# Performance work log

Measured on AMD Instinct MI355X. Metric: run time of the kernel, lower is better.

## Reference

```python
import jax, jax.numpy as jnp
import numpy as np

N = 50000      # nodes
E = 800000     # edges
H = 64         # hid_dim (== in_dim)
T = 4          # number of S2V message-passing steps


def setup_inputs() -> dict:
    key = jax.random.key(0)
    ks = jax.random.split(key, 12)
    mu = jax.random.normal(ks[0], (N, H), dtype=jnp.float32)
    x = jax.random.uniform(ks[1], (N, 1), dtype=jnp.float32)
    edge_index = jax.random.randint(ks[2], (2, E), 0, N, dtype=jnp.int64)
    edge_w = jax.random.uniform(ks[3], (E, 1), dtype=jnp.float32)
    s = 0.05  # small init scale to keep activations bounded across T relu layers
    W1 = jax.random.normal(ks[4], (T, H, 1), dtype=jnp.float32) * s   # lin1 per layer, torch [out,in]
    W2 = jax.random.normal(ks[5], (T, H, H), dtype=jnp.float32) * s   # lin2 per layer
    W3 = jax.random.normal(ks[6], (T, H, H), dtype=jnp.float32) * s   # lin3 per layer
    W4 = jax.random.normal(ks[7], (T, H, 1), dtype=jnp.float32) * s   # lin4 per layer
    W5 = jax.random.normal(ks[8], (1, 2 * H), dtype=jnp.float32) * s  # lin5
    W7 = jax.random.normal(ks[9], (H, H), dtype=jnp.float32) * s      # lin7
    return {"mu": mu, "x": x, "edge_index": edge_index, "edge_w": edge_w,
            "W1": W1, "W2": W2, "W3": W3, "W4": W4, "W5": W5, "W7": W7}


def _s2v_step(mu, x, idx, edge_w, w1, w2, w3, w4):
    # Faithful to source: gather AND scatter both use edge_index[1].
    x_emb = x @ w1.T                                            # [N,H]
    mu_j = mu[idx]                                              # [E,H] gather
    mu_aggr = jax.ops.segment_sum(mu_j, idx, num_segments=N)    # [N,H] scatter_add
    mu_aggr = mu_aggr @ w2.T
    ew = jax.nn.relu(edge_w @ w4.T)                             # [E,H]
    ew_aggr = jax.ops.segment_sum(ew, idx, num_segments=N)      # [N,H]
    ew_aggr = ew_aggr @ w3.T
    return jax.nn.relu(x_emb + mu_aggr + ew_aggr)


def reference(mu, x, edge_index, edge_w, W1, W2, W3, W4, W5, W7):
    idx = edge_index[1]
    for t in range(T):
        mu = _s2v_step(mu, x, idx, edge_w, W1[t], W2[t], W3[t], W4[t])
    nodes_vec = mu @ W7.T                                       # [N,H]
    graph_pool = jnp.broadcast_to(jnp.sum(mu, axis=0, keepdims=True), (N, H))
    cat = jnp.concatenate([graph_pool, nodes_vec], axis=1)      # [N,2H]
    return (jax.nn.relu(cat) @ W5.T).squeeze(-1)                # [N]
```

## Files before the change

kernel.cpp:

```cpp
#include <hip/hip_runtime.h>

#define H 64
#define NPB 64
#define KS 104
typedef short bf16x8 __attribute__((ext_vector_type(8)));
typedef float f32x4 __attribute__((ext_vector_type(4)));

static __device__ __forceinline__ unsigned short f2bf(float f) {
    union { float f; unsigned u; } v; v.f = f;
    unsigned r = v.u + 0x7fffu + ((v.u >> 16) & 1u);
    return (unsigned short)(r >> 16);
}
static __device__ __forceinline__ float bf2f(unsigned short b) {
    union { unsigned u; float f; } v; v.u = ((unsigned)b) << 16;
    return v.f;
}
static __device__ __forceinline__ void split8(const float* ff, bf16x8& hi, bf16x8& lo) {
#pragma unroll
    for (int j = 0; j < 8; ++j) {
        unsigned short h = f2bf(ff[j]);
        hi[j] = (short)h;
        lo[j] = (short)f2bf(ff[j] - bf2f(h));
    }
}


__global__ __launch_bounds__(256)
void edge_prep_kernel(const int* __restrict__ ei, const float* __restrict__ ew,
                      const float* __restrict__ W1, const float* __restrict__ W2,
                      const float* __restrict__ W3, const float* __restrict__ W4,
                      const float* __restrict__ W7, float* __restrict__ dSf,
                      bf16x8* __restrict__ Bp, bf16x8* __restrict__ W7p, int E) {
    __shared__ float v3s[256];
    const int t = threadIdx.x;
    const int bid = blockIdx.x;

    if (bid == 0) {
        {
            int tl = t >> 6, h2 = t & 63;
            const float* __restrict__ w3r = W3 + (tl * H + h2) * H;
            const float* __restrict__ w4r = W4 + tl * H;
            float a0 = 0, a1 = 0, a2 = 0, a3 = 0;
#pragma unroll
            for (int k = 0; k < H; k += 4) {
                a0 += fmaxf(w4r[k + 0], 0.f) * w3r[k + 0];
                a1 += fmaxf(w4r[k + 1], 0.f) * w3r[k + 1];
                a2 += fmaxf(w4r[k + 2], 0.f) * w3r[k + 2];
                a3 += fmaxf(w4r[k + 3], 0.f) * w3r[k + 3];
            }
            v3s[t] = (a0 + a1) + (a2 + a3);
        }
        __syncthreads();
        const int w = t >> 6, lane = t & 63, c = lane & 15, q = lane >> 4;
        const int hh = 16 * w + c;
        for (int tl = 0; tl < 4; ++tl) {
            const int b3 = (tl * 4 + w) * 3;
            bf16x8 hi, lo;
#pragma unroll
            for (int s = 0; s < 2; ++s) {
                const float* __restrict__ wp = W2 + (tl * H + hh) * H + s * 32 + q * 8;
                float4 f0 = *(const float4*)(wp);
                float4 f1 = *(const float4*)(wp + 4);
                float ff[8] = {f0.x, f0.y, f0.z, f0.w, f1.x, f1.y, f1.z, f1.w};
                split8(ff, hi, lo);
                Bp[(b3 + s) * 128 + lane] = hi;
                Bp[(b3 + s) * 128 + 64 + lane] = lo;
            }
            float ff[8] = {0, 0, 0, 0, 0, 0, 0, 0};
            if (q == 0) { ff[0] = W1[tl * H + hh]; ff[1] = v3s[tl * H + hh]; }
            split8(ff, hi, lo);
            Bp[(b3 + 2) * 128 + lane] = hi;
            Bp[(b3 + 2) * 128 + 64 + lane] = lo;
        }
#pragma unroll
        for (int s = 0; s < 2; ++s) {
            const float* __restrict__ wp = W7 + hh * H + s * 32 + q * 8;
            float4 f0 = *(const float4*)(wp);
            float4 f1 = *(const float4*)(wp + 4);
            float ff[8] = {f0.x, f0.y, f0.z, f0.w, f1.x, f1.y, f1.z, f1.w};
            bf16x8 hi, lo;
            split8(ff, hi, lo);
            W7p[(w * 2 + s) * 128 + lane] = hi;
            W7p[(w * 2 + s) * 128 + 64 + lane] = lo;
        }
        return;
    }

    int probe = ei[2 * (t & 63) + 1];
    bool is64 = (__ballot(probe != 0) == 0ULL);
    const int base_e = 8 * ((bid - 1) * 256 + t);
#pragma unroll
    for (int g = 0; g < 2; ++g) {
        int e0 = base_e + 4 * g;
        if (e0 + 3 < E) {
            float4 wv = *(const float4*)(ew + e0);
            int i0, i1, i2, i3;
            if (is64) {
                int4 a = *(const int4*)(ei + 2 * (E + e0));
                int4 b = *(const int4*)(ei + 2 * (E + e0) + 4);
                i0 = a.x; i1 = a.z; i2 = b.x; i3 = b.z;
            } else {
                int4 a = *(const int4*)(ei + E + e0);
                i0 = a.x; i1 = a.y; i2 = a.z; i3 = a.w;
            }
            unsafeAtomicAdd(&dSf[i0], 4096.0f + wv.x);
            unsafeAtomicAdd(&dSf[i1], 4096.0f + wv.y);
            unsafeAtomicAdd(&dSf[i2], 4096.0f + wv.z);
            unsafeAtomicAdd(&dSf[i3], 4096.0f + wv.w);
        } else {
            for (int j = 0; j < 4 && e0 + j < E; ++j) {
                int e = e0 + j;
                int idx = is64 ? ei[2 * (E + e)] : ei[E + e];
                unsafeAtomicAdd(&dSf[idx], 4096.0f + ew[e]);
            }
        }
    }
}

__global__ __launch_bounds__(256, 4)
void node_kernel(const float* __restrict__ mu, const float* __restrict__ x,
                 const float* __restrict__ W5, const bf16x8* __restrict__ Bp,
                 const bf16x8* __restrict__ W7p, const float* __restrict__ dSf,
                 float* __restrict__ gp, float* __restrict__ out, int N) {
    __shared__ unsigned short Ab[2][NPB * KS];
    __shared__ float degs[NPB];
    __shared__ float red[4 * NPB];

    const int t = threadIdx.x;
    const int lane = t & 63;
    const int w = __builtin_amdgcn_readfirstlane(t >> 6);
    const int c = lane & 15;
    const int q = lane >> 4;
    const int hh = 16 * w + c;
    const int base = blockIdx.x * NPB;

    if (t < 128) {
        int buf = t >> 6, row = t & 63;
        unsigned* p = (unsigned*)&Ab[buf][row * KS];
#pragma unroll
        for (int d = 33; d < 52; ++d) p[d] = 0u;
    }
    if (t < 64) {
        int node = base + t;
        float dg = 0.f, sv = 0.f, xv = 0.f;
        if (node < N) {
            float T = dSf[node];
            float k = floorf(T * (1.0f / 4096.0f));
            dg = k;
            sv = T - 4096.0f * k;
            xv = x[node];
        }
        degs[t] = dg;
        unsigned short xb = f2bf(xv), sb = f2bf(sv);
        Ab[0][t * KS + 64] = xb; Ab[0][t * KS + 65] = sb;
        Ab[1][t * KS + 64] = xb; Ab[1][t * KS + 65] = sb;
    }
    __syncthreads();

    {
        const float* __restrict__ mublk = mu + (size_t)base * H;
        const int maxf = (N - base) * H;
#pragma unroll
        for (int cc = 0; cc < 4; ++cc) {
            int f = (t + 256 * cc) * 4;
            float4 v = make_float4(0.f, 0.f, 0.f, 0.f);
            if (f < maxf) v = *(const float4*)(mublk + f);
            int m = f >> 6, k = f & 63;
            float dg = degs[m];
            ushort4 b;
            b.x = f2bf(v.x * dg); b.y = f2bf(v.y * dg);
            b.z = f2bf(v.z * dg); b.w = f2bf(v.w * dg);
            *(ushort4*)(&Ab[0][m * KS + k]) = b;
        }
    }
    __syncthreads();

    unsigned short* Acur = &Ab[0][0];
    unsigned short* Anxt = &Ab[1][0];

    for (int tl = 0; tl < 4; ++tl) {
        const int b3 = (tl * 4 + w) * 3;
        bf16x8 bh0 = Bp[(b3 + 0) * 128 + lane], bl0 = Bp[(b3 + 0) * 128 + 64 + lane];
        bf16x8 bh1 = Bp[(b3 + 1) * 128 + lane], bl1 = Bp[(b3 + 1) * 128 + 64 + lane];
        bf16x8 bh2 = Bp[(b3 + 2) * 128 + lane], bl2 = Bp[(b3 + 2) * 128 + 64 + lane];

        f32x4 acc[4];
#pragma unroll
        for (int mt = 0; mt < 4; ++mt)
#pragma unroll
            for (int r = 0; r < 4; ++r) acc[mt][r] = 0.f;

#pragma unroll
        for (int mt = 0; mt < 4; ++mt) {
            const unsigned short* ar = Acur + (mt * 16 + c) * KS;
            bf16x8 a0 = *(const bf16x8*)(ar + q * 8);
            bf16x8 a1 = *(const bf16x8*)(ar + 32 + q * 8);
            bf16x8 a2 = *(const bf16x8*)(ar + 64 + q * 8);
            acc[mt] = __builtin_amdgcn_mfma_f32_16x16x32_bf16(a0, bh0, acc[mt], 0, 0, 0);
            acc[mt] = __builtin_amdgcn_mfma_f32_16x16x32_bf16(a0, bl0, acc[mt], 0, 0, 0);
            acc[mt] = __builtin_amdgcn_mfma_f32_16x16x32_bf16(a1, bh1, acc[mt], 0, 0, 0);
            acc[mt] = __builtin_amdgcn_mfma_f32_16x16x32_bf16(a1, bl1, acc[mt], 0, 0, 0);
            acc[mt] = __builtin_amdgcn_mfma_f32_16x16x32_bf16(a2, bh2, acc[mt], 0, 0, 0);
            acc[mt] = __builtin_amdgcn_mfma_f32_16x16x32_bf16(a2, bl2, acc[mt], 0, 0, 0);
        }

        const bool scale = (tl < 3);
#pragma unroll
        for (int mt = 0; mt < 4; ++mt) {
#pragma unroll
            for (int r = 0; r < 4; ++r) {
                int m = mt * 16 + q * 4 + r;
                float v = fmaxf(acc[mt][r], 0.f);
                if (scale) v *= degs[m];
                Anxt[m * KS + hh] = f2bf(v);
            }
        }
        __syncthreads();
        unsigned short* tmp = Acur; Acur = Anxt; Anxt = tmp;
    }

    {
        bf16x8 bh0 = W7p[(w * 2 + 0) * 128 + lane], bl0 = W7p[(w * 2 + 0) * 128 + 64 + lane];
        bf16x8 bh1 = W7p[(w * 2 + 1) * 128 + lane], bl1 = W7p[(w * 2 + 1) * 128 + 64 + lane];
        f32x4 acc[4];
#pragma unroll
        for (int mt = 0; mt < 4; ++mt)
#pragma unroll
            for (int r = 0; r < 4; ++r) acc[mt][r] = 0.f;
#pragma unroll
        for (int mt = 0; mt < 4; ++mt) {
            const unsigned short* ar = Acur + (mt * 16 + c) * KS;
            bf16x8 a0 = *(const bf16x8*)(ar + q * 8);
            bf16x8 a1 = *(const bf16x8*)(ar + 32 + q * 8);
            acc[mt] = __builtin_amdgcn_mfma_f32_16x16x32_bf16(a0, bh0, acc[mt], 0, 0, 0);
            acc[mt] = __builtin_amdgcn_mfma_f32_16x16x32_bf16(a0, bl0, acc[mt], 0, 0, 0);
            acc[mt] = __builtin_amdgcn_mfma_f32_16x16x32_bf16(a1, bh1, acc[mt], 0, 0, 0);
            acc[mt] = __builtin_amdgcn_mfma_f32_16x16x32_bf16(a1, bl1, acc[mt], 0, 0, 0);
        }
        float w5v = W5[H + hh];
#pragma unroll
        for (int mt = 0; mt < 4; ++mt) {
#pragma unroll
            for (int r = 0; r < 4; ++r) {
                float v = fmaxf(acc[mt][r], 0.f) * w5v;
                v += __shfl_xor(v, 1);
                v += __shfl_xor(v, 2);
                v += __shfl_xor(v, 4);
                v += __shfl_xor(v, 8);
                if (c == 0) red[w * 64 + mt * 16 + q * 4 + r] = v;
            }
        }
    }
    __syncthreads();
    if (t < 64) {
        float pn = red[t] + red[64 + t] + red[128 + t] + red[192 + t];
        if (base + t < N) out[base + t] = pn;
    }
    __syncthreads();

    {
        int h2 = t & 63, mq = t >> 6;
        float s = 0.f;
#pragma unroll
        for (int i = 0; i < 16; ++i) s += bf2f(Acur[(mq * 16 + i) * KS + h2]);
        red[t] = s;
    }
    __syncthreads();
    if (t < 64) {
        float g = red[t] + red[64 + t] + red[128 + t] + red[192 + t];
        unsafeAtomicAdd(&gp[t], g);
    }
}

__global__ __launch_bounds__(256)
void finalize_kernel(const float* __restrict__ gp, const float* __restrict__ W5,
                     float* __restrict__ out, int N) {
    int lane = threadIdx.x & 63;
    float v = fmaxf(gp[lane], 0.f) * W5[lane];
    v += __shfl_xor(v, 1);
    v += __shfl_xor(v, 2);
    v += __shfl_xor(v, 4);
    v += __shfl_xor(v, 8);
    v += __shfl_xor(v, 16);
    v += __shfl_xor(v, 32);
    int n = blockIdx.x * blockDim.x + threadIdx.x;
    if (n < N) out[n] += v;
}

extern "C" void kernel_launch(void* const* d_in, const int* in_sizes, int n_in,
                              void* d_out, int out_size, void* d_ws, size_t ws_size,
                              hipStream_t stream) {
    const float* mu = (const float*)d_in[0];
    const float* x  = (const float*)d_in[1];
    const int*   ei = (const int*)d_in[2];
    const float* ew = (const float*)d_in[3];
    const float* W1 = (const float*)d_in[4];
    const float* W2 = (const float*)d_in[5];
    const float* W3 = (const float*)d_in[6];
    const float* W4 = (const float*)d_in[7];
    const float* W5 = (const float*)d_in[8];
    const float* W7 = (const float*)d_in[9];
    float* out = (float*)d_out;

    const int N = in_sizes[1];
    const int E = in_sizes[3];

    char* ws = (char*)d_ws;
    float*  dSf = (float*)ws;
    float*  gp  = (float*)(ws + (size_t)N * 4);
    bf16x8* Bp  = (bf16x8*)(ws + (size_t)N * 4 + 256);
    bf16x8* W7p = (bf16x8*)(ws + (size_t)N * 4 + 256 + 196608);

    hipMemsetAsync(ws, 0, (size_t)N * 4 + 256, stream);

    int nb_e = 1 + (E + 8 * 256 - 1) / (8 * 256);
    edge_prep_kernel<<<nb_e, 256, 0, stream>>>(ei, ew, W1, W2, W3, W4, W7,
                                               dSf, Bp, W7p, E);
    node_kernel<<<(N + NPB - 1) / NPB, 256, 0, stream>>>(mu, x, W5, Bp, W7p,
                                                         dSf, gp, out, N);
    finalize_kernel<<<(N + 255) / 256, 256, 0, stream>>>(gp, W5, out, N);
}
```

Baseline: 154.5 us.

## Keep node activations in registers with transposed MFMA, drop shared-memory staging

The node kernel now computes the transposed product (weights times activations), so each wave keeps its own 16 nodes' activations in MFMA B-operand registers across all four layers. Activations are re-laid out between layers with lane shuffles instead of being written to LDS and reloaded behind a block barrier. The x*W1 and edge-weight terms are applied as scalar FMAs in the epilogue rather than as a third K-slice of the MFMA, which removes two MFMAs per tile. This cuts LDS traffic, block barriers and the LDS footprint, at the cost of more shuffles, more registers, and repeated small global loads of W1/v3 per layer.

```diff
diff --git a/kernel.cpp b/kernel.cpp
--- a/kernel.cpp
+++ b/kernel.cpp
@@ -2,7 +2,6 @@
 
 #define H 64
 #define NPB 64
-#define KS 104
 typedef short bf16x8 __attribute__((ext_vector_type(8)));
 typedef float f32x4 __attribute__((ext_vector_type(4)));
 
@@ -14,6 +13,9 @@
 static __device__ __forceinline__ float bf2f(unsigned short b) {
     union { unsigned u; float f; } v; v.u = ((unsigned)b) << 16;
     return v.f;
+}
+static __device__ __forceinline__ unsigned pack2bf(float a, float b) {
+    return (unsigned)f2bf(a) | ((unsigned)f2bf(b) << 16);
 }
 static __device__ __forceinline__ void split8(const float* ff, bf16x8& hi, bf16x8& lo) {
 #pragma unroll
@@ -30,7 +32,8 @@
                       const float* __restrict__ W1, const float* __restrict__ W2,
                       const float* __restrict__ W3, const float* __restrict__ W4,
                       const float* __restrict__ W7, float* __restrict__ dSf,
-                      bf16x8* __restrict__ Bp, bf16x8* __restrict__ W7p, int E) {
+                      float* __restrict__ v3g, bf16x8* __restrict__ Wp,
+                      bf16x8* __restrict__ W7p, int E) {
     __shared__ float v3s[256];
     const int t = threadIdx.x;
     const int bid = blockIdx.x;
@@ -51,37 +54,33 @@
             v3s[t] = (a0 + a1) + (a2 + a3);
         }
         __syncthreads();
-        const int w = t >> 6, lane = t & 63, c = lane & 15, q = lane >> 4;
-        const int hh = 16 * w + c;
-        for (int tl = 0; tl < 4; ++tl) {
-            const int b3 = (tl * 4 + w) * 3;
-            bf16x8 hi, lo;
-#pragma unroll
-            for (int s = 0; s < 2; ++s) {
-                const float* __restrict__ wp = W2 + (tl * H + hh) * H + s * 32 + q * 8;
-                float4 f0 = *(const float4*)(wp);
-                float4 f1 = *(const float4*)(wp + 4);
-                float ff[8] = {f0.x, f0.y, f0.z, f0.w, f1.x, f1.y, f1.z, f1.w};
-                split8(ff, hi, lo);
-                Bp[(b3 + s) * 128 + lane] = hi;
-                Bp[(b3 + s) * 128 + 64 + lane] = lo;
-            }
-            float ff[8] = {0, 0, 0, 0, 0, 0, 0, 0};
-            if (q == 0) { ff[0] = W1[tl * H + hh]; ff[1] = v3s[tl * H + hh]; }
-            split8(ff, hi, lo);
-            Bp[(b3 + 2) * 128 + lane] = hi;
-            Bp[(b3 + 2) * 128 + 64 + lane] = lo;
-        }
-#pragma unroll
-        for (int s = 0; s < 2; ++s) {
-            const float* __restrict__ wp = W7 + hh * H + s * 32 + q * 8;
+        v3g[t] = v3s[t];
+        const int lane = t & 63, set = t >> 6, c = lane & 15, q = lane >> 4;
+#pragma unroll
+        for (int it = 0; it < 8; ++it) {
+            int combo = it * 4 + set;
+            int tl = combo >> 3, ht = (combo >> 1) & 3, ks = combo & 1;
+            const float* __restrict__ wp = W2 + ((tl * 4 + ht) * 16 + c) * 64 + ks * 32 + q * 8;
             float4 f0 = *(const float4*)(wp);
             float4 f1 = *(const float4*)(wp + 4);
             float ff[8] = {f0.x, f0.y, f0.z, f0.w, f1.x, f1.y, f1.z, f1.w};
             bf16x8 hi, lo;
             split8(ff, hi, lo);
-            W7p[(w * 2 + s) * 128 + lane] = hi;
-            W7p[(w * 2 + s) * 128 + 64 + lane] = lo;
+            Wp[(combo * 2 + 0) * 64 + lane] = hi;
+            Wp[(combo * 2 + 1) * 64 + lane] = lo;
+        }
+#pragma unroll
+        for (int it = 0; it < 2; ++it) {
+            int combo = it * 4 + set;
+            int ht = combo >> 1, ks = combo & 1;
+            const float* __restrict__ wp = W7 + (ht * 16 + c) * 64 + ks * 32 + q * 8;
+            float4 f0 = *(const float4*)(wp);
+            float4 f1 = *(const float4*)(wp + 4);
+            float ff[8] = {f0.x, f0.y, f0.z, f0.w, f1.x, f1.y, f1.z, f1.w};
+            bf16x8 hi, lo;
+            split8(ff, hi, lo);
+            W7p[(combo * 2 + 0) * 64 + lane] = hi;
+            W7p[(combo * 2 + 1) * 64 + lane] = lo;
         }
         return;
     }
@@ -119,155 +118,156 @@
 
 __global__ __launch_bounds__(256, 4)
 void node_kernel(const float* __restrict__ mu, const float* __restrict__ x,
-                 const float* __restrict__ W5, const bf16x8* __restrict__ Bp,
+                 const float* __restrict__ W1, const float* __restrict__ W5,
+                 const float* __restrict__ v3g, const bf16x8* __restrict__ Wp,
                  const bf16x8* __restrict__ W7p, const float* __restrict__ dSf,
                  float* __restrict__ gp, float* __restrict__ out, int N) {
-    __shared__ unsigned short Ab[2][NPB * KS];
-    __shared__ float degs[NPB];
-    __shared__ float red[4 * NPB];
+    __shared__ float gpr[4 * 64];
 
     const int t = threadIdx.x;
     const int lane = t & 63;
-    const int w = __builtin_amdgcn_readfirstlane(t >> 6);
+    const int wv = __builtin_amdgcn_readfirstlane(t >> 6);
     const int c = lane & 15;
     const int q = lane >> 4;
-    const int hh = 16 * w + c;
-    const int base = blockIdx.x * NPB;
-
-    if (t < 128) {
-        int buf = t >> 6, row = t & 63;
-        unsigned* p = (unsigned*)&Ab[buf][row * KS];
-#pragma unroll
-        for (int d = 33; d < 52; ++d) p[d] = 0u;
-    }
-    if (t < 64) {
-        int node = base + t;
-        float dg = 0.f, sv = 0.f, xv = 0.f;
-        if (node < N) {
-            float T = dSf[node];
-            float k = floorf(T * (1.0f / 4096.0f));
-            dg = k;
-            sv = T - 4096.0f * k;
-            xv = x[node];
-        }
-        degs[t] = dg;
-        unsigned short xb = f2bf(xv), sb = f2bf(sv);
-        Ab[0][t * KS + 64] = xb; Ab[0][t * KS + 65] = sb;
-        Ab[1][t * KS + 64] = xb; Ab[1][t * KS + 65] = sb;
-    }
-    __syncthreads();
-
+    const int node = blockIdx.x * NPB + wv * 16 + c;
+    const bool valid = node < N;
+
+    float dg = 0.f, sv = 0.f, xv = 0.f;
+    if (valid) {
+        float T = dSf[node];
+        dg = floorf(T * (1.0f / 4096.0f));
+        sv = T - 4096.0f * dg;
+        xv = x[node];
+    }
+
+    bf16x8 B0, B1;
     {
-        const float* __restrict__ mublk = mu + (size_t)base * H;
-        const int maxf = (N - base) * H;
-#pragma unroll
-        for (int cc = 0; cc < 4; ++cc) {
-            int f = (t + 256 * cc) * 4;
-            float4 v = make_float4(0.f, 0.f, 0.f, 0.f);
-            if (f < maxf) v = *(const float4*)(mublk + f);
-            int m = f >> 6, k = f & 63;
-            float dg = degs[m];
-            ushort4 b;
-            b.x = f2bf(v.x * dg); b.y = f2bf(v.y * dg);
-            b.z = f2bf(v.z * dg); b.w = f2bf(v.w * dg);
-            *(ushort4*)(&Ab[0][m * KS + k]) = b;
-        }
-    }
-    __syncthreads();
-
-    unsigned short* Acur = &Ab[0][0];
-    unsigned short* Anxt = &Ab[1][0];
-
+        float ff0[8] = {0,0,0,0,0,0,0,0}, ff1[8] = {0,0,0,0,0,0,0,0};
+        if (valid) {
+            const float* __restrict__ mp = mu + (size_t)node * H + q * 8;
+            float4 a0 = *(const float4*)(mp);
+            float4 a1 = *(const float4*)(mp + 4);
+            float4 b0 = *(const float4*)(mp + 32);
+            float4 b1 = *(const float4*)(mp + 36);
+            float t0[8] = {a0.x, a0.y, a0.z, a0.w, a1.x, a1.y, a1.z, a1.w};
+            float t1[8] = {b0.x, b0.y, b0.z, b0.w, b1.x, b1.y, b1.z, b1.w};
+#pragma unroll
+            for (int j = 0; j < 8; ++j) { ff0[j] = t0[j] * dg; ff1[j] = t1[j] * dg; }
+        }
+#pragma unroll
+        for (int j = 0; j < 8; ++j) { B0[j] = (short)f2bf(ff0[j]); B1[j] = (short)f2bf(ff1[j]); }
+    }
+
+    unsigned pk[4][2];
+    const int lo_lane = 32 * (q & 1) + c;
+    const bool hsel = ((q >> 1) != 0);
+
+#pragma unroll
     for (int tl = 0; tl < 4; ++tl) {
-        const int b3 = (tl * 4 + w) * 3;
-        bf16x8 bh0 = Bp[(b3 + 0) * 128 + lane], bl0 = Bp[(b3 + 0) * 128 + 64 + lane];
-        bf16x8 bh1 = Bp[(b3 + 1) * 128 + lane], bl1 = Bp[(b3 + 1) * 128 + 64 + lane];
-        bf16x8 bh2 = Bp[(b3 + 2) * 128 + lane], bl2 = Bp[(b3 + 2) * 128 + 64 + lane];
-
         f32x4 acc[4];
 #pragma unroll
-        for (int mt = 0; mt < 4; ++mt)
-#pragma unroll
-            for (int r = 0; r < 4; ++r) acc[mt][r] = 0.f;
-
-#pragma unroll
-        for (int mt = 0; mt < 4; ++mt) {
-            const unsigned short* ar = Acur + (mt * 16 + c) * KS;
-            bf16x8 a0 = *(const bf16x8*)(ar + q * 8);
-            bf16x8 a1 = *(const bf16x8*)(ar + 32 + q * 8);
-            bf16x8 a2 = *(const bf16x8*)(ar + 64 + q * 8);
-            acc[mt] = __builtin_amdgcn_mfma_f32_16x16x32_bf16(a0, bh0, acc[mt], 0, 0, 0);
-            acc[mt] = __builtin_amdgcn_mfma_f32_16x16x32_bf16(a0, bl0, acc[mt], 0, 0, 0);
-            acc[mt] = __builtin_amdgcn_mfma_f32_16x16x32_bf16(a1, bh1, acc[mt], 0, 0, 0);
-            acc[mt] = __builtin_amdgcn_mfma_f32_16x16x32_bf16(a1, bl1, acc[mt], 0, 0, 0);
-            acc[mt] = __builtin_amdgcn_mfma_f32_16x16x32_bf16(a2, bh2, acc[mt], 0, 0, 0);
-            acc[mt] = __builtin_amdgcn_mfma_f32_16x16x32_bf16(a2, bl2, acc[mt], 0, 0, 0);
-        }
-
+        for (int ht = 0; ht < 4; ++ht) {
+            const int e0 = (tl * 8 + ht * 2) * 2;
+            bf16x8 h0 = Wp[(e0 + 0) * 64 + lane];
+            bf16x8 l0 = Wp[(e0 + 1) * 64 + lane];
+            bf16x8 h1 = Wp[(e0 + 2) * 64 + lane];
+            bf16x8 l1 = Wp[(e0 + 3) * 64 + lane];
+            f32x4 a = {0.f, 0.f, 0.f, 0.f};
+            a = __builtin_amdgcn_mfma_f32_16x16x32_bf16(h0, B0, a, 0, 0, 0);
+            a = __builtin_amdgcn_mfma_f32_16x16x32_bf16(l0, B0, a, 0, 0, 0);
+            a = __builtin_amdgcn_mfma_f32_16x16x32_bf16(h1, B1, a, 0, 0, 0);
+            a = __builtin_amdgcn_mfma_f32_16x16x32_bf16(l1, B1, a, 0, 0, 0);
+            acc[ht] = a;
+        }
         const bool scale = (tl < 3);
 #pragma unroll
-        for (int mt = 0; mt < 4; ++mt) {
-#pragma unroll
-            for (int r = 0; r < 4; ++r) {
-                int m = mt * 16 + q * 4 + r;
-                float v = fmaxf(acc[mt][r], 0.f);
-                if (scale) v *= degs[m];
-                Anxt[m * KS + hh] = f2bf(v);
-            }
-        }
-        __syncthreads();
-        unsigned short* tmp = Acur; Acur = Anxt; Anxt = tmp;
+        for (int ht = 0; ht < 4; ++ht) {
+            float4 w1f = *(const float4*)(W1 + tl * 64 + ht * 16 + q * 4);
+            float4 v3f = *(const float4*)(v3g + tl * 64 + ht * 16 + q * 4);
+            float v0 = fmaxf(xv * w1f.x + acc[ht][0] + sv * v3f.x, 0.f);
+            float v1 = fmaxf(xv * w1f.y + acc[ht][1] + sv * v3f.y, 0.f);
+            float v2 = fmaxf(xv * w1f.z + acc[ht][2] + sv * v3f.z, 0.f);
+            float v3 = fmaxf(xv * w1f.w + acc[ht][3] + sv * v3f.w, 0.f);
+            if (scale) { v0 *= dg; v1 *= dg; v2 *= dg; v3 *= dg; }
+            pk[ht][0] = pack2bf(v0, v1);
+            pk[ht][1] = pack2bf(v2, v3);
+        }
+        {
+            union { unsigned u[4]; bf16x8 v; } cv;
+            unsigned a0 = (unsigned)__shfl((int)pk[0][0], lo_lane);
+            unsigned b0 = (unsigned)__shfl((int)pk[1][0], lo_lane);
+            unsigned a1 = (unsigned)__shfl((int)pk[0][1], lo_lane);
+            unsigned b1 = (unsigned)__shfl((int)pk[1][1], lo_lane);
+            unsigned a2 = (unsigned)__shfl((int)pk[0][0], lo_lane + 16);
+            unsigned b2 = (unsigned)__shfl((int)pk[1][0], lo_lane + 16);
+            unsigned a3 = (unsigned)__shfl((int)pk[0][1], lo_lane + 16);
+            unsigned b3 = (unsigned)__shfl((int)pk[1][1], lo_lane + 16);
+            cv.u[0] = hsel ? b0 : a0;
+            cv.u[1] = hsel ? b1 : a1;
+            cv.u[2] = hsel ? b2 : a2;
+            cv.u[3] = hsel ? b3 : a3;
+            B0 = cv.v;
+            a0 = (unsigned)__shfl((int)pk[2][0], lo_lane);
+            b0 = (unsigned)__shfl((int)pk[3][0], lo_lane);
+            a1 = (unsigned)__shfl((int)pk[2][1], lo_lane);
+            b1 = (unsigned)__shfl((int)pk[3][1], lo_lane);
+            a2 = (unsigned)__shfl((int)pk[2][0], lo_lane + 16);
+            b2 = (unsigned)__shfl((int)pk[3][0], lo_lane + 16);
+            a3 = (unsigned)__shfl((int)pk[2][1], lo_lane + 16);
+            b3 = (unsigned)__shfl((int)pk[3][1], lo_lane + 16);
+            cv.u[0] = hsel ? b0 : a0;
+            cv.u[1] = hsel ? b1 : a1;
+            cv.u[2] = hsel ? b2 : a2;
+            cv.u[3] = hsel ? b3 : a3;
+            B1 = cv.v;
+        }
     }
 
     {
-        bf16x8 bh0 = W7p[(w * 2 + 0) * 128 + lane], bl0 = W7p[(w * 2 + 0) * 128 + 64 + lane];
-        bf16x8 bh1 = W7p[(w * 2 + 1) * 128 + lane], bl1 = W7p[(w * 2 + 1) * 128 + 64 + lane];
         f32x4 acc[4];
 #pragma unroll
-        for (int mt = 0; mt < 4; ++mt)
-#pragma unroll
-            for (int r = 0; r < 4; ++r) acc[mt][r] = 0.f;
-#pragma unroll
-        for (int mt = 0; mt < 4; ++mt) {
-            const unsigned short* ar = Acur + (mt * 16 + c) * KS;
-            bf16x8 a0 = *(const bf16x8*)(ar + q * 8);
-            bf16x8 a1 = *(const bf16x8*)(ar + 32 + q * 8);
-            acc[mt] = __builtin_amdgcn_mfma_f32_16x16x32_bf16(a0, bh0, acc[mt], 0, 0, 0);
-            acc[mt] = __builtin_amdgcn_mfma_f32_16x16x32_bf16(a0, bl0, acc[mt], 0, 0, 0);
-            acc[mt] = __builtin_amdgcn_mfma_f32_16x16x32_bf16(a1, bh1, acc[mt], 0, 0, 0);
-            acc[mt] = __builtin_amdgcn_mfma_f32_16x16x32_bf16(a1, bl1, acc[mt], 0, 0, 0);
-        }
-        float w5v = W5[H + hh];
-#pragma unroll
-        for (int mt = 0; mt < 4; ++mt) {
-#pragma unroll
-            for (int r = 0; r < 4; ++r) {
-                float v = fmaxf(acc[mt][r], 0.f) * w5v;
-                v += __shfl_xor(v, 1);
-                v += __shfl_xor(v, 2);
-                v += __shfl_xor(v, 4);
-                v += __shfl_xor(v, 8);
-                if (c == 0) red[w * 64 + mt * 16 + q * 4 + r] = v;
-            }
+        for (int ht = 0; ht < 4; ++ht) {
+            const int e0 = (ht * 2) * 2;
+            bf16x8 h0 = W7p[(e0 + 0) * 64 + lane];
+            bf16x8 l0 = W7p[(e0 + 1) * 64 + lane];
+            bf16x8 h1 = W7p[(e0 + 2) * 64 + lane];
+            bf16x8 l1 = W7p[(e0 + 3) * 64 + lane];
+            f32x4 a = {0.f, 0.f, 0.f, 0.f};
+            a = __builtin_amdgcn_mfma_f32_16x16x32_bf16(h0, B0, a, 0, 0, 0);
+            a = __builtin_amdgcn_mfma_f32_16x16x32_bf16(l0, B0, a, 0, 0, 0);
+            a = __builtin_amdgcn_mfma_f32_16x16x32_bf16(h1, B1, a, 0, 0, 0);
+            a = __builtin_amdgcn_mfma_f32_16x16x32_bf16(l1, B1, a, 0, 0, 0);
+            acc[ht] = a;
+        }
+        float pn = 0.f;
+#pragma unroll
+        for (int ht = 0; ht < 4; ++ht) {
+            float4 w5f = *(const float4*)(W5 + 64 + ht * 16 + q * 4);
+            pn += fmaxf(acc[ht][0], 0.f) * w5f.x;
+            pn += fmaxf(acc[ht][1], 0.f) * w5f.y;
+            pn += fmaxf(acc[ht][2], 0.f) * w5f.z;
+            pn += fmaxf(acc[ht][3], 0.f) * w5f.w;
+        }
+        pn += __shfl_xor(pn, 16);
+        pn += __shfl_xor(pn, 32);
+        if (valid && q == 0) out[node] = pn;
+    }
+
+#pragma unroll
+    for (int ht = 0; ht < 4; ++ht) {
+#pragma unroll
+        for (int r = 0; r < 4; ++r) {
+            float m = bf2f((unsigned short)(pk[ht][r >> 1] >> ((r & 1) * 16)));
+            m += __shfl_xor(m, 1);
+            m += __shfl_xor(m, 2);
+            m += __shfl_xor(m, 4);
+            m += __shfl_xor(m, 8);
+            if (c == 0) gpr[wv * 64 + ht * 16 + q * 4 + r] = m;
         }
     }
     __syncthreads();
     if (t < 64) {
-        float pn = red[t] + red[64 + t] + red[128 + t] + red[192 + t];
-        if (base + t < N) out[base + t] = pn;
-    }
-    __syncthreads();
-
-    {
-        int h2 = t & 63, mq = t >> 6;
-        float s = 0.f;
-#pragma unroll
-        for (int i = 0; i < 16; ++i) s += bf2f(Acur[(mq * 16 + i) * KS + h2]);
-        red[t] = s;
-    }
-    __syncthreads();
-    if (t < 64) {
-        float g = red[t] + red[64 + t] + red[128 + t] + red[192 + t];
+        float g = gpr[t] + gpr[64 + t] + gpr[128 + t] + gpr[192 + t];
         unsafeAtomicAdd(&gp[t], g);
     }
 }
@@ -308,15 +308,16 @@
     char* ws = (char*)d_ws;
     float*  dSf = (float*)ws;
     float*  gp  = (float*)(ws + (size_t)N * 4);
-    bf16x8* Bp  = (bf16x8*)(ws + (size_t)N * 4 + 256);
-    bf16x8* W7p = (bf16x8*)(ws + (size_t)N * 4 + 256 + 196608);
+    float*  v3g = (float*)(ws + (size_t)N * 4 + 256);
+    bf16x8* Wp  = (bf16x8*)(ws + (size_t)N * 4 + 1280);
+    bf16x8* W7p = (bf16x8*)(ws + (size_t)N * 4 + 1280 + 65536);
 
     hipMemsetAsync(ws, 0, (size_t)N * 4 + 256, stream);
 
     int nb_e = 1 + (E + 8 * 256 - 1) / (8 * 256);
     edge_prep_kernel<<<nb_e, 256, 0, stream>>>(ei, ew, W1, W2, W3, W4, W7,
-                                               dSf, Bp, W7p, E);
-    node_kernel<<<(N + NPB - 1) / NPB, 256, 0, stream>>>(mu, x, W5, Bp, W7p,
-                                                         dSf, gp, out, N);
+                                               dSf, v3g, Wp, W7p, E);
+    node_kernel<<<(N + NPB - 1) / NPB, 256, 0, stream>>>(mu, x, W1, W5, v3g,
+                                                         Wp, W7p, dSf, gp, out, N);
     finalize_kernel<<<(N + 255) / 256, 256, 0, stream>>>(gp, W5, out, N);
 }
```

Result: slower. 159.9 us (+3.5%).
